# Kernel tuning notes

Hardware: AMD Instinct MI355X
Metric: run time of the kernel (lower is better)

Reference implementation:

```python
import jax, jax.numpy as jnp
import numpy as np

V, H, L, NH, DH, FF, P, T = 21128, 768, 12, 12, 64, 3072, 512, 9
B, S = 16, 256
EPS = 1e-12

def _ln(x, g, b):
    m = x.mean(-1, keepdims=True)
    v = ((x - m) ** 2).mean(-1, keepdims=True)
    return (x - m) * jax.lax.rsqrt(v + EPS) * g + b

def setup_inputs() -> dict:
    key = jax.random.key(0)
    ks = iter(jax.random.split(key, 64))
    def nrm(shape, s=0.02):
        return (jax.random.normal(next(ks), shape, jnp.float32) * s)
    inp = {
        'input_ids': jax.random.randint(next(ks), (B, 1, S), 0, V, dtype=jnp.int32),
        'token_type_ids': jnp.zeros((B, 1, S), jnp.int32),
        'attention_mask': jnp.ones((B, 1, S), jnp.int32),
        'tags': jax.random.randint(next(ks), (B, S), 0, T, dtype=jnp.int32),
        'word_emb': nrm((V, H)), 'pos_emb': nrm((P, H)), 'type_emb': nrm((2, H)),
        'emb_ln_g': jnp.ones((H,), jnp.float32), 'emb_ln_b': jnp.zeros((H,), jnp.float32),
        'Wq': nrm((L, H, H)), 'bq': jnp.zeros((L, H), jnp.float32),
        'Wk': nrm((L, H, H)), 'bk': jnp.zeros((L, H), jnp.float32),
        'Wv': nrm((L, H, H)), 'bv': jnp.zeros((L, H), jnp.float32),
        'Wo': nrm((L, H, H)), 'bo': jnp.zeros((L, H), jnp.float32),
        'ln1_g': jnp.ones((L, H), jnp.float32), 'ln1_b': jnp.zeros((L, H), jnp.float32),
        'W1': nrm((L, H, FF)), 'b1': jnp.zeros((L, FF), jnp.float32),
        'W2': nrm((L, FF, H)), 'b2': jnp.zeros((L, H), jnp.float32),
        'ln2_g': jnp.ones((L, H), jnp.float32), 'ln2_b': jnp.zeros((L, H), jnp.float32),
        'dense_W': nrm((H, T)), 'dense_b': jnp.zeros((T,), jnp.float32),
        'crf_start': nrm((T,), 0.1), 'crf_end': nrm((T,), 0.1), 'crf_trans': nrm((T, T), 0.1),
    }
    return inp

def _model(input_ids, token_type_ids, attention_mask, tags,
           word_emb, pos_emb, type_emb, emb_ln_g, emb_ln_b,
           Wq, bq, Wk, bk, Wv, bv, Wo, bo, ln1_g, ln1_b,
           W1, b1, W2, b2, ln2_g, ln2_b, dense_W, dense_b,
           crf_start, crf_end, crf_trans):
    ids = input_ids[:, 0, :]            # [B,S]
    tt = token_type_ids[:, 0, :]
    amask = attention_mask[:, 0, :]     # [B,S] int
    Bn, Sn = ids.shape
    # --- BERT embeddings (post-LN BERT-base) ---
    x = word_emb[ids] + pos_emb[:Sn][None, :, :] + type_emb[tt]
    x = _ln(x, emb_ln_g, emb_ln_b)
    bias = jnp.where(amask[:, None, None, :] > 0, 0.0, -1e9).astype(x.dtype)  # [B,1,1,S]
    scale = 1.0 / np.sqrt(DH).astype(np.float32)
    def layer(h, p):
        wq, bq_, wk, bk_, wv, bv_, wo, bo_, g1, c1, w1, d1, w2, d2, g2, c2 = p
        q = (h @ wq + bq_).reshape(Bn, Sn, NH, DH).transpose(0, 2, 1, 3)
        k = (h @ wk + bk_).reshape(Bn, Sn, NH, DH).transpose(0, 2, 1, 3)
        v = (h @ wv + bv_).reshape(Bn, Sn, NH, DH).transpose(0, 2, 1, 3)
        att = jax.nn.softmax(jnp.einsum('bhqd,bhkd->bhqk', q, k) * scale + bias, axis=-1)
        ctx = jnp.einsum('bhqk,bhkd->bhqd', att, v).transpose(0, 2, 1, 3).reshape(Bn, Sn, H)
        h = _ln(h + ctx @ wo + bo_, g1, c1)
        ff = jax.nn.gelu(h @ w1 + d1, approximate=False)
        h = _ln(h + ff @ w2 + d2, g2, c2)
        return h, None
    x, _ = jax.lax.scan(layer, x, (Wq, bq, Wk, bk, Wv, bv, Wo, bo, ln1_g, ln1_b, W1, b1, W2, b2, ln2_g, ln2_b))
    # --- emission head, seq-first like the torch code ---
    emis = (x @ dense_W + dense_b).transpose(1, 0, 2)   # [S,B,T]
    m = (amask.T > 0)                                    # [S,B] bool
    tags_sb = tags.T                                     # [S,B]
    bidx = jnp.arange(Bn)
    # --- CRF numerator (gold path score) ---
    score0 = crf_start[tags_sb[0]] + emis[0, bidx, tags_sb[0]]
    def num_step(sc, inp):
        e, t, tp, mm = inp
        inc = crf_trans[tp, t] + e[bidx, t]
        return sc + jnp.where(mm, inc, 0.0), None
    score, _ = jax.lax.scan(num_step, score0, (emis[1:], tags_sb[1:], tags_sb[:-1], m[1:]))
    lengths = m.astype(jnp.int32).sum(0)                 # [B]
    last_tag = jnp.take_along_axis(tags_sb, (lengths - 1)[None, :], axis=0)[0]
    score = score + crf_end[last_tag]
    # --- CRF partition (forward algorithm) ---
    alpha0 = crf_start[None, :] + emis[0]                # [B,T]
    def fwd_step(a, inp):
        e, mm = inp
        nxt = jax.nn.logsumexp(a[:, :, None] + crf_trans[None, :, :] + e[:, None, :], axis=1)
        return jnp.where(mm[:, None], nxt, a), None
    alpha, _ = jax.lax.scan(fwd_step, alpha0, (emis[1:], m[1:]))
    logZ = jax.nn.logsumexp(alpha + crf_end[None, :], axis=-1)
    loss = -(score - logZ).mean()                        # reduction='mean'
    # --- Viterbi decode ---
    v0 = crf_start[None, :] + emis[0]
    tid = jnp.arange(T)
    def vit_step(vv, inp):
        e, mm = inp
        sc = vv[:, :, None] + crf_trans[None, :, :]       # [B,T,T]
        nv = sc.max(1) + e
        idx = sc.argmax(1).astype(jnp.int32)
        vv2 = jnp.where(mm[:, None], nv, vv)
        idx = jnp.where(mm[:, None], idx, tid[None, :].astype(jnp.int32))
        return vv2, idx
    vfin, hist = jax.lax.scan(vit_step, v0, (emis[1:], m[1:]))  # hist: [S-1,B,T]
    last = jnp.argmax(vfin + crf_end[None, :], axis=-1).astype(jnp.int32)  # [B]
    def back_step(t, h):
        prev = jnp.take_along_axis(h, t[:, None], axis=1)[:, 0]
        return prev, prev
    _, path = jax.lax.scan(back_step, last, hist, reverse=True)  # [S-1,B]
    preds = jnp.concatenate([path, last[None, :]], axis=0).T     # [B,S]
    return loss, preds

def reference(input_ids, token_type_ids, attention_mask, tags,
              word_emb, pos_emb, type_emb, emb_ln_g, emb_ln_b,
              Wq, bq, Wk, bk, Wv, bv, Wo, bo, ln1_g, ln1_b,
              W1, b1, W2, b2, ln2_g, ln2_b, dense_W, dense_b,
              crf_start, crf_end, crf_trans):
    return _model(input_ids, token_type_ids, attention_mask, tags,
                  word_emb, pos_emb, type_emb, emb_ln_g, emb_ln_b,
                  Wq, bq, Wk, bk, Wv, bv, Wo, bo, ln1_g, ln1_b,
                  W1, b1, W2, b2, ln2_g, ln2_b, dense_W, dense_b,
                  crf_start, crf_end, crf_trans)
```

## Files before the change

### kernel.cpp

```cpp
#include <hip/hip_runtime.h>
#include <math.h>

#define B_ 16
#define S_ 256
#define H_ 768
#define L_ 12
#define NH_ 12
#define DH_ 64
#define FF_ 3072
#define T_ 9

typedef unsigned short ushort_t;
typedef __attribute__((ext_vector_type(8))) __bf16 bf16x8;
typedef __attribute__((ext_vector_type(4))) float f32x4;
typedef __attribute__((ext_vector_type(4))) unsigned short us4;
typedef __attribute__((ext_vector_type(4))) unsigned int u32x4;

__device__ __forceinline__ ushort_t f2bf(float f) {
  union { float f; unsigned u; } v; v.f = f;
  unsigned r = v.u + 0x7FFFu + ((v.u >> 16) & 1u);
  return (ushort_t)(r >> 16);
}
__device__ __forceinline__ float bf2f(ushort_t h) {
  union { unsigned u; float f; } v; v.u = ((unsigned)h) << 16;
  return v.f;
}
__device__ __forceinline__ void gload16(const void* g, void* l) {
  __builtin_amdgcn_global_load_lds((const __attribute__((address_space(1))) void*)g,
                                   (__attribute__((address_space(3))) void*)l, 16, 0, 0);
}

__global__ __launch_bounds__(256) void emb_ln_kernel(const int* __restrict__ ids, const int* __restrict__ tt,
                              const float* __restrict__ we, const float* __restrict__ pe,
                              const float* __restrict__ te, const float* __restrict__ g,
                              const float* __restrict__ bb, float* __restrict__ out,
                              ushort_t* __restrict__ oh, ushort_t* __restrict__ ol) {
  const int token = blockIdx.x;
  const int tid = threadIdx.x;
  const int s = token & (S_ - 1);
  const int id = ids[token];
  const int t2 = tt[token];
  float x[3];
  float sum = 0.f;
#pragma unroll
  for (int i = 0; i < 3; ++i) {
    int d = tid + i * 256;
    x[i] = we[(size_t)id * H_ + d] + pe[(size_t)s * H_ + d] + te[(size_t)t2 * H_ + d];
    sum += x[i];
  }
  __shared__ float red[4];
#pragma unroll
  for (int o = 32; o > 0; o >>= 1) sum += __shfl_xor(sum, o, 64);
  const int wid = tid >> 6, lane = tid & 63;
  if (lane == 0) red[wid] = sum;
  __syncthreads();
  const float mean = (red[0] + red[1] + red[2] + red[3]) * (1.f / H_);
  float vs = 0.f;
#pragma unroll
  for (int i = 0; i < 3; ++i) { float dv = x[i] - mean; vs += dv * dv; }
#pragma unroll
  for (int o = 32; o > 0; o >>= 1) vs += __shfl_xor(vs, o, 64);
  __syncthreads();
  if (lane == 0) red[wid] = vs;
  __syncthreads();
  const float var = (red[0] + red[1] + red[2] + red[3]) * (1.f / H_);
  const float inv = rsqrtf(var + 1e-12f);
  float* op = out + (size_t)token * H_;
  ushort_t* hp = oh + (size_t)token * H_;
  ushort_t* lp = ol + (size_t)token * H_;
#pragma unroll
  for (int i = 0; i < 3; ++i) {
    int d = tid + i * 256;
    float y = (x[i] - mean) * inv * g[d] + bb[d];
    op[d] = y;
    ushort_t h = f2bf(y);
    hp[d] = h;
    lp[d] = f2bf(y - bf2f(h));
  }
}

__global__ __launch_bounds__(256) void ln_kernel(const float* __restrict__ base, const float* __restrict__ delta,
                          const float* __restrict__ g, const float* __restrict__ bb,
                          float* __restrict__ out, ushort_t* __restrict__ oh, ushort_t* __restrict__ ol) {
  const int token = blockIdx.x;
  const int tid = threadIdx.x;
  const float* bp = base + (size_t)token * H_;
  const float* dp = delta + (size_t)token * H_;
  float x[3];
  float s = 0.f;
#pragma unroll
  for (int i = 0; i < 3; ++i) { int d = tid + i * 256; x[i] = bp[d] + dp[d]; s += x[i]; }
  __shared__ float red[4];
#pragma unroll
  for (int o = 32; o > 0; o >>= 1) s += __shfl_xor(s, o, 64);
  const int wid = tid >> 6, lane = tid & 63;
  if (lane == 0) red[wid] = s;
  __syncthreads();
  const float mean = (red[0] + red[1] + red[2] + red[3]) * (1.f / H_);
  float vs = 0.f;
#pragma unroll
  for (int i = 0; i < 3; ++i) { float dv = x[i] - mean; vs += dv * dv; }
#pragma unroll
  for (int o = 32; o > 0; o >>= 1) vs += __shfl_xor(vs, o, 64);
  __syncthreads();
  if (lane == 0) red[wid] = vs;
  __syncthreads();
  const float var = (red[0] + red[1] + red[2] + red[3]) * (1.f / H_);
  const float inv = rsqrtf(var + 1e-12f);
  float* op = out + (size_t)token * H_;
  ushort_t* hp = oh + (size_t)token * H_;
  ushort_t* lp = ol + (size_t)token * H_;
#pragma unroll
  for (int i = 0; i < 3; ++i) {
    int d = tid + i * 256;
    float y = (x[i] - mean) * inv * g[d] + bb[d];
    op[d] = y;
    ushort_t h = f2bf(y);
    hp[d] = h;
    lp[d] = f2bf(y - bf2f(h));
  }
}

__device__ __forceinline__ void transpose_core(float (*t)[65], const float* __restrict__ src,
                                               ushort_t* __restrict__ dh,
                                               int K, int N, int n0, int k0) {
  const int tid = threadIdx.x;
#pragma unroll
  for (int i = 0; i < 16; ++i) {
    int lin = tid + i * 256;
    int kk = lin >> 6, nn = lin & 63;
    t[kk][nn] = src[(size_t)(k0 + kk) * N + n0 + nn];
  }
  __syncthreads();
#pragma unroll
  for (int i = 0; i < 16; ++i) {
    int lin = tid + i * 256;
    int nn = lin >> 6, kk = lin & 63;
    dh[(size_t)(n0 + nn) * K + k0 + kk] = f2bf(t[kk][nn]);
  }
}

__device__ __forceinline__ void wprep_dispatch(float (*t)[65], int wid,
                        const float* Wq, const float* Wk, const float* Wv, const float* Wo,
                        const float* W1, const float* W2,
                        ushort_t* WT4h, ushort_t* W1th, ushort_t* W2th) {
  if (wid < 576) {
    const int z = wid / 144, r = wid - z * 144;
    const int x = r % 12, y = r / 12;
    const float* src = z == 0 ? Wq : (z == 1 ? Wk : (z == 2 ? Wv : Wo));
    transpose_core(t, src, WT4h + (size_t)z * H_ * H_, H_, H_, x * 64, y * 64);
  } else if (wid < 1152) {
    const int i = wid - 576;
    const int x = i % 48, y = i / 48;
    transpose_core(t, W1, W1th, H_, FF_, x * 64, y * 64);
  } else {
    const int i = wid - 1152;
    const int x = i % 12, y = i / 12;
    transpose_core(t, W2, W2th, FF_, H_, x * 64, y * 64);
  }
}

__global__ __launch_bounds__(256) void wprep_k(const float* __restrict__ Wq, const float* __restrict__ Wk,
                        const float* __restrict__ Wv, const float* __restrict__ Wo,
                        const float* __restrict__ W1, const float* __restrict__ W2,
                        ushort_t* __restrict__ WT4h,
                        ushort_t* __restrict__ W1th, ushort_t* __restrict__ W2th) {
  __shared__ float t[64][65];
  wprep_dispatch(t, blockIdx.x, Wq, Wk, Wv, Wo, W1, W2, WT4h, W1th, W2th);
}

template <int R>
__device__ __forceinline__ void stage_slice(const ushort_t* __restrict__ gsrc, int K, char* lds) {
  const int tid = threadIdx.x;
  constexpr int NIT = (R * 4) / 256;
#pragma unroll
  for (int i = 0; i < NIT; ++i) {
    const int v = tid + i * 256;
    const int kh = v / (2 * R);
    const int r2 = v & (2 * R - 1);
    const int row = r2 >> 1;
    const int kg = (kh << 1) | ((r2 & 1) ^ ((row >> 2) & 1));
    gload16(gsrc + (size_t)row * K + kg * 8, lds + (i * 256 + (tid & 192)) * 16);
  }
}
template <int R>
__device__ __forceinline__ void stage64(const ushort_t* __restrict__ gsrc, int K, char* lds) {
  stage_slice<R>(gsrc, K, lds);
  stage_slice<R>(gsrc + 32, K, lds + R * 64);
}

template <int BM, int BN>
__device__ __forceinline__ void mgemm_acc(
    const ushort_t* __restrict__ Ah, const ushort_t* __restrict__ Al,
    const ushort_t* __restrict__ Bth,
    int K, f32x4 (&acc)[BM / 32][BN / 32],
    ushort_t* sAh, ushort_t* sAl, ushort_t* sBh) {
  constexpr int FM = BM / 32;
  constexpr int FN = BN / 32;
  const int tid = threadIdx.x;
  const int w = tid >> 6, lane = tid & 63;
  const int wm = w >> 1, wn = w & 1;
  const int kgL = lane >> 4, lr = lane & 15;
  const int row0 = blockIdx.y * BM, col0 = blockIdx.x * BN;

#pragma unroll
  for (int i = 0; i < FM; ++i)
#pragma unroll
    for (int j = 0; j < FN; ++j) acc[i][j] = (f32x4){0.f, 0.f, 0.f, 0.f};

  const int khL = kgL >> 1;
  const int swz = (((kgL & 1) ^ ((lr >> 2) & 1)) << 4);
  const int aB0 = khL * (BM * 32) + (wm * (BM / 2) + lr) * 32 + swz;
  const int bB0 = khL * (BN * 32) + (wn * (BN / 2) + lr) * 32 + swz;

  const ushort_t* gA_h = Ah + (size_t)row0 * K;
  const ushort_t* gA_l = Al + (size_t)row0 * K;
  const ushort_t* gB_h = Bth + (size_t)col0 * K;

  for (int k0 = 0; k0 < K; k0 += 64) {
    stage64<BM>(gA_h + k0, K, (char*)sAh);
    stage64<BM>(gA_l + k0, K, (char*)sAl);
    stage64<BN>(gB_h + k0, K, (char*)sBh);
    __syncthreads();

#pragma unroll
    for (int ks = 0; ks < 2; ++ks) {
      const int ao = ks * BM * 64 + aB0;
      const int bo = ks * BN * 64 + bB0;
      bf16x8 a_h[FM], a_l[FM], b_h[FN];
#pragma unroll
      for (int fm = 0; fm < FM; ++fm) {
        a_h[fm] = *(const bf16x8*)((const char*)sAh + ao + fm * 512);
        a_l[fm] = *(const bf16x8*)((const char*)sAl + ao + fm * 512);
      }
#pragma unroll
      for (int fn = 0; fn < FN; ++fn) {
        b_h[fn] = *(const bf16x8*)((const char*)sBh + bo + fn * 512);
      }
#pragma unroll
      for (int fm = 0; fm < FM; ++fm)
#pragma unroll
        for (int fn = 0; fn < FN; ++fn) {
          f32x4 c = acc[fm][fn];
          c = __builtin_amdgcn_mfma_f32_16x16x32_bf16(a_h[fm], b_h[fn], c, 0, 0, 0);
          c = __builtin_amdgcn_mfma_f32_16x16x32_bf16(a_l[fm], b_h[fn], c, 0, 0, 0);
          acc[fm][fn] = c;
        }
    }
    __syncthreads();
  }
}

template <int BM, int BN, int EPI>
__global__ __launch_bounds__(256) void mgemm(const ushort_t* __restrict__ Ah, const ushort_t* __restrict__ Al,
                      const ushort_t* __restrict__ Bth,
                      const float* __restrict__ bias, float* __restrict__ Cf,
                      ushort_t* __restrict__ Ch, ushort_t* __restrict__ Cl, int N, int K) {
  __shared__ __attribute__((aligned(16))) ushort_t sAh[BM * 64];
  __shared__ __attribute__((aligned(16))) ushort_t sAl[BM * 64];
  __shared__ __attribute__((aligned(16))) ushort_t sBh[BN * 64];
  f32x4 acc[BM / 32][BN / 32];
  mgemm_acc<BM, BN>(Ah, Al, Bth, K, acc, sAh, sAl, sBh);
  const int tid = threadIdx.x;
  const int w = tid >> 6, lane = tid & 63;
  const int wm = w >> 1, wn = w & 1;
  const int kg = lane >> 4, lr = lane & 15;
  const int row0 = blockIdx.y * BM, col0 = blockIdx.x * BN;
#pragma unroll
  for (int fn = 0; fn < BN / 32; ++fn) {
    const int col = col0 + wn * (BN / 2) + fn * 16 + lr;
    const float bv = bias[col];
#pragma unroll
    for (int fm = 0; fm < BM / 32; ++fm) {
#pragma unroll
      for (int r = 0; r < 4; ++r) {
        const int row = row0 + wm * (BM / 2) + fm * 16 + kg * 4 + r;
        float v = acc[fm][fn][r] + bv;
        if (EPI == 0) {
          Cf[(size_t)row * N + col] = v;
        } else {
          float gl = 0.5f * v * (1.f + erff(v * 0.70710678118654752f));
          ushort_t h = f2bf(gl);
          Ch[(size_t)row * N + col] = h;
          Cl[(size_t)row * N + col] = f2bf(gl - bf2f(h));
        }
      }
    }
  }
}

__global__ __launch_bounds__(256) void ff1_fused(
    const ushort_t* __restrict__ Xh, const ushort_t* __restrict__ Xl,
    const ushort_t* __restrict__ W1th, const float* __restrict__ bias,
    ushort_t* __restrict__ Ch, ushort_t* __restrict__ Cl,
    const float* __restrict__ WqN, const float* __restrict__ WkN,
    const float* __restrict__ WvN, const float* __restrict__ WoN,
    const float* __restrict__ W1N, const float* __restrict__ W2N,
    ushort_t* __restrict__ WT4hN, ushort_t* __restrict__ W1thN, ushort_t* __restrict__ W2thN) {
  __shared__ __attribute__((aligned(16))) char pool[128 * 64 * 2 * 3];
  if (blockIdx.y >= 32) {
    if (WqN == nullptr) return;
    const int wid = (blockIdx.y - 32) * 24 + blockIdx.x;
    wprep_dispatch((float(*)[65])pool, wid, WqN, WkN, WvN, WoN, W1N, W2N, WT4hN, W1thN, W2thN);
    return;
  }
  ushort_t* sAh = (ushort_t*)pool;
  ushort_t* sAl = sAh + 128 * 64;
  ushort_t* sBh = sAl + 128 * 64;
  f32x4 acc[4][4];
  mgemm_acc<128, 128>(Xh, Xl, W1th, H_, acc, sAh, sAl, sBh);
  const int tid = threadIdx.x;
  const int w = tid >> 6, lane = tid & 63;
  const int wm = w >> 1, wn = w & 1;
  const int kg = lane >> 4, lr = lane & 15;
  const int row0 = blockIdx.y * 128, col0 = blockIdx.x * 128;
#pragma unroll
  for (int fn = 0; fn < 4; ++fn) {
    const int col = col0 + wn * 64 + fn * 16 + lr;
    const float bv = bias[col];
#pragma unroll
    for (int fm = 0; fm < 4; ++fm) {
#pragma unroll
      for (int r = 0; r < 4; ++r) {
        const int row = row0 + wm * 64 + fm * 16 + kg * 4 + r;
        float v = acc[fm][fn][r] + bv;
        float gl = 0.5f * v * (1.f + erff(v * 0.70710678118654752f));
        ushort_t h = f2bf(gl);
        Ch[(size_t)row * FF_ + col] = h;
        Cl[(size_t)row * FF_ + col] = f2bf(gl - bf2f(h));
      }
    }
  }
}

__global__ __launch_bounds__(256) void qkv_m(const ushort_t* __restrict__ Xh, const ushort_t* __restrict__ Xl,
                      const ushort_t* __restrict__ WT4h,
                      const float* __restrict__ bq, const float* __restrict__ bk,
                      const float* __restrict__ bvv,
                      ushort_t* __restrict__ Qh, ushort_t* __restrict__ Ql,
                      ushort_t* __restrict__ Kh, ushort_t* __restrict__ Vth) {
  __shared__ __attribute__((aligned(16))) ushort_t sAh[128 * 64];
  __shared__ __attribute__((aligned(16))) ushort_t sAl[128 * 64];
  __shared__ __attribute__((aligned(16))) ushort_t sBh[128 * 64];
  const int z = blockIdx.z;
  const ushort_t* Bh = WT4h + (size_t)z * H_ * H_;
  const float* bias = z == 0 ? bq : (z == 1 ? bk : bvv);
  f32x4 acc[4][4];
  mgemm_acc<128, 128>(Xh, Xl, Bh, H_, acc, sAh, sAl, sBh);
  const int tid = threadIdx.x;
  const int w = tid >> 6, lane = tid & 63;
  const int wm = w >> 1, wn = w & 1;
  const int kg = lane >> 4, lr = lane & 15;
  const int row0 = blockIdx.y * 128, col0 = blockIdx.x * 128;
#pragma unroll
  for (int fn = 0; fn < 4; ++fn) {
    const int col = col0 + wn * 64 + fn * 16 + lr;
    const float bv = bias[col];
#pragma unroll
    for (int fm = 0; fm < 4; ++fm) {
      const int rowb = row0 + wm * 64 + fm * 16 + kg * 4;
      if (z == 0) {
#pragma unroll
        for (int r = 0; r < 4; ++r) {
          float v = acc[fm][fn][r] + bv;
          ushort_t h = f2bf(v);
          Qh[(size_t)(rowb + r) * H_ + col] = h;
          Ql[(size_t)(rowb + r) * H_ + col] = f2bf(v - bf2f(h));
        }
      } else if (z == 1) {
#pragma unroll
        for (int r = 0; r < 4; ++r) {
          Kh[(size_t)(rowb + r) * H_ + col] = f2bf(acc[fm][fn][r] + bv);
        }
      } else {
        us4 h4;
#pragma unroll
        for (int r = 0; r < 4; ++r) h4[r] = f2bf(acc[fm][fn][r] + bv);
        const int bb2 = rowb >> 8, s0 = rowb & 255;
        const int hh2 = col >> 6, d = col & 63;
        *(us4*)(Vth + ((size_t)(bb2 * NH_ + hh2) * DH_ + d) * S_ + s0) = h4;
      }
    }
  }
}

__global__ __launch_bounds__(256, 3) void attn_mfma(
    const ushort_t* __restrict__ Qh, const ushort_t* __restrict__ Ql,
    const ushort_t* __restrict__ Kh, const ushort_t* __restrict__ Vth,
    const int* __restrict__ amask,
    ushort_t* __restrict__ Oh, ushort_t* __restrict__ Ol) {
  const int bid = blockIdx.x;
  const int qt = bid / 192;
  const int gh = bid - qt * 192;
  const int b = gh / NH_;
  const int h = gh - b * NH_;
  __shared__ __attribute__((aligned(16))) ushort_t sKh[64 * 64];
  __shared__ __attribute__((aligned(16))) ushort_t sVh[64 * 64];
  __shared__ __attribute__((aligned(16))) unsigned sP[4][16 * 68];
  __shared__ float sBias[64];
  const int tid = threadIdx.x;
  const int w = tid >> 6, lane = tid & 63;
  const int kg = lane >> 4, lr = lane & 15;

  const int qrow = b * S_ + qt * 64 + w * 16 + lr;
  bf16x8 qfh[2], qfl[2];
#pragma unroll
  for (int ds2 = 0; ds2 < 2; ++ds2) {
    const size_t off = (size_t)qrow * H_ + h * DH_ + ds2 * 32 + kg * 8;
    qfh[ds2] = *(const bf16x8*)(Qh + off);
    qfl[ds2] = *(const bf16x8*)(Ql + off);
  }

  f32x4 ctx[4];
#pragma unroll
  for (int i = 0; i < 4; ++i) ctx[i] = (f32x4){0.f, 0.f, 0.f, 0.f};
  float mrow[4], lrw[4];
#pragma unroll
  for (int r = 0; r < 4; ++r) { mrow[r] = -1e30f; lrw[r] = 0.f; }

  unsigned* sPw = &sP[w][0];

  for (int kt = 0; kt < 4; ++kt) {
#pragma unroll
    for (int i = 0; i < 2; ++i) {
      const int v = tid + i * 256;
      const int row = v >> 3;
      const int c16 = (v & 7) ^ (row & 7);
      const size_t kgl = (size_t)(b * S_ + kt * 64 + row) * H_ + h * DH_ + c16 * 8;
      gload16(Kh + kgl, (char*)sKh + v * 16);
      const size_t vgl = (size_t)((b * NH_ + h) * DH_ + row) * S_ + kt * 64 + c16 * 8;
      gload16(Vth + vgl, (char*)sVh + v * 16);
    }
    if (tid < 64) sBias[tid] = (amask[b * S_ + kt * 64 + tid] > 0) ? 0.f : -1e9f;
    __syncthreads();

    f32x4 sc[4];
#pragma unroll
    for (int kf = 0; kf < 4; ++kf) sc[kf] = (f32x4){0.f, 0.f, 0.f, 0.f};
#pragma unroll
    for (int kf = 0; kf < 4; ++kf) {
      const int krow = kf * 16 + lr;
#pragma unroll
      for (int ds2 = 0; ds2 < 2; ++ds2) {
        const int cb = (ds2 * 64 + kg * 16) ^ ((krow & 7) << 4);
        const bf16x8 kvh = *(const bf16x8*)((const char*)sKh + krow * 128 + cb);
        sc[kf] = __builtin_amdgcn_mfma_f32_16x16x32_bf16(qfh[ds2], kvh, sc[kf], 0, 0, 0);
        sc[kf] = __builtin_amdgcn_mfma_f32_16x16x32_bf16(qfl[ds2], kvh, sc[kf], 0, 0, 0);
      }
    }
    float bsv[4];
#pragma unroll
    for (int kf = 0; kf < 4; ++kf) bsv[kf] = sBias[kf * 16 + lr];

#pragma unroll
    for (int r = 0; r < 4; ++r) {
      float sv[4];
      float tmax = -1e30f;
#pragma unroll
      for (int kf = 0; kf < 4; ++kf) {
        sv[kf] = sc[kf][r] * 0.125f + bsv[kf];
        tmax = fmaxf(tmax, sv[kf]);
      }
#pragma unroll
      for (int o = 8; o > 0; o >>= 1) tmax = fmaxf(tmax, __shfl_xor(tmax, o, 64));
      const float mnew = fmaxf(mrow[r], tmax);
      const float corr = expf(mrow[r] - mnew);
      float ls = 0.f;
      const int qoff = (kg * 4 + r) * 68;
#pragma unroll
      for (int kf = 0; kf < 4; ++kf) {
        const float pe = expf(sv[kf] - mnew);
        ls += pe;
        const ushort_t hi = f2bf(pe);
        const ushort_t lo = f2bf(pe - bf2f(hi));
        sPw[qoff + kf * 16 + lr] = ((unsigned)hi << 16) | lo;
      }
#pragma unroll
      for (int o = 8; o > 0; o >>= 1) ls += __shfl_xor(ls, o, 64);
      lrw[r] = lrw[r] * corr + ls;
      mrow[r] = mnew;
#pragma unroll
      for (int df = 0; df < 4; ++df) ctx[df][r] *= corr;
    }

#pragma unroll
    for (int ks = 0; ks < 2; ++ks) {
      unsigned w8[8];
      *(u32x4*)&w8[0] = *(const u32x4*)(sPw + lr * 68 + ks * 32 + kg * 8);
      *(u32x4*)&w8[4] = *(const u32x4*)(sPw + lr * 68 + ks * 32 + kg * 8 + 4);
      union { bf16x8 v; ushort_t u[8]; } ph, pl;
#pragma unroll
      for (int j = 0; j < 8; ++j) { ph.u[j] = (ushort_t)(w8[j] >> 16); pl.u[j] = (ushort_t)(w8[j] & 0xffffu); }
#pragma unroll
      for (int df = 0; df < 4; ++df) {
        const int vrow = df * 16 + lr;
        const int cb = (ks * 64 + kg * 16) ^ ((vrow & 7) << 4);
        const bf16x8 vvh = *(const bf16x8*)((const char*)sVh + vrow * 128 + cb);
        ctx[df] = __builtin_amdgcn_mfma_f32_16x16x32_bf16(ph.v, vvh, ctx[df], 0, 0, 0);
        ctx[df] = __builtin_amdgcn_mfma_f32_16x16x32_bf16(pl.v, vvh, ctx[df], 0, 0, 0);
      }
    }
    __syncthreads();
  }

#pragma unroll
  for (int r = 0; r < 4; ++r) {
    const float inv = 1.f / lrw[r];
    const int tok = b * S_ + qt * 64 + w * 16 + kg * 4 + r;
#pragma unroll
    for (int df = 0; df < 4; ++df) {
      const float v = ctx[df][r] * inv;
      const ushort_t hi = f2bf(v);
      const size_t o = (size_t)tok * H_ + h * DH_ + df * 16 + lr;
      Oh[o] = hi;
      Ol[o] = f2bf(v - bf2f(hi));
    }
  }
}

__global__ __launch_bounds__(256) void emis_kernel(const float* __restrict__ X, const float* __restrict__ W,
                            const float* __restrict__ bias, float* __restrict__ E) {
  const int wave = (blockIdx.x * 256 + threadIdx.x) >> 6;
  const int lane = threadIdx.x & 63;
  const int b = wave >> 8, s = wave & 255;
  const float* xp = X + (size_t)wave * H_;
  float acc[T_];
#pragma unroll
  for (int t = 0; t < T_; ++t) acc[t] = 0.f;
  for (int i = 0; i < 12; ++i) {
    const int d = lane + i * 64;
    const float xv = xp[d];
    const float* wp = W + (size_t)d * T_;
#pragma unroll
    for (int t = 0; t < T_; ++t) acc[t] = fmaf(xv, wp[t], acc[t]);
  }
#pragma unroll
  for (int t = 0; t < T_; ++t) {
    float v = acc[t];
#pragma unroll
    for (int o = 32; o > 0; o >>= 1) v += __shfl_xor(v, o, 64);
    acc[t] = v;
  }
  if (lane < T_) E[((size_t)s * B_ + b) * T_ + lane] = acc[lane] + bias[lane];
}

__global__ __launch_bounds__(128) void crf_kernel(const float* __restrict__ emis, const int* __restrict__ tags,
                          const int* __restrict__ amask,
                          const float* __restrict__ crf_start, const float* __restrict__ crf_end,
                          const float* __restrict__ trans,
                          float* __restrict__ partial, float* __restrict__ out) {
  const int b = blockIdx.x;
  const int tid = threadIdx.x;
  const int wv = tid >> 6;
  const int lane = tid & 63;
  __shared__ float sE[S_ * T_];
  __shared__ float sM[S_];
  __shared__ float trs[T_ * T_];
  __shared__ unsigned char hist[S_ - 1][16];
  __shared__ float pathf[S_];
  for (int i = tid; i < S_ * T_; i += 128) {
    const int s = i / T_, t = i - s * T_;
    sE[i] = emis[((size_t)s * B_ + b) * T_ + t];
  }
  for (int i = tid; i < S_; i += 128) sM[i] = (float)amask[b * S_ + i];
  for (int i = tid; i < T_ * T_; i += 128) trs[i] = trans[i];
  __syncthreads();

  const int t = lane;
  const bool act = t < T_;
  float trc[T_];
#pragma unroll
  for (int p = 0; p < T_; ++p) trc[p] = act ? trs[p * T_ + t] : 0.f;

  if (wv == 0) {
    float alpha = act ? crf_start[t] + sE[t] : 0.f;
    for (int s = 1; s < S_; ++s) {
      float ap[T_];
#pragma unroll
      for (int p = 0; p < T_; ++p) ap[p] = __shfl(alpha, p, 64);
      if (act) {
        const float e = sE[s * T_ + t];
        float mx = -1e30f;
#pragma unroll
        for (int p = 0; p < T_; ++p) mx = fmaxf(mx, ap[p] + trc[p]);
        float sum = 0.f;
#pragma unroll
        for (int p = 0; p < T_; ++p) sum += __expf(ap[p] + trc[p] - mx);
        const float na = mx + __logf(sum) + e;
        if (sM[s] > 0.f) alpha = na;
      }
    }
    float nsum = 0.f;
    int len = 0;
#pragma unroll
    for (int j = 0; j < 4; ++j) {
      const int s = lane + j * 64;
      const int mk = (sM[s] > 0.f) ? 1 : 0;
      len += mk;
      if (s >= 1 && mk) {
        const int tc = tags[b * S_ + s], tp = tags[b * S_ + s - 1];
        nsum += trs[tp * T_ + tc] + sE[s * T_ + tc];
      }
    }
#pragma unroll
    for (int o = 32; o > 0; o >>= 1) {
      nsum += __shfl_xor(nsum, o, 64);
      len += __shfl_xor(len, o, 64);
    }
    const float fz = act ? alpha + crf_end[t] : -1e30f;
    float zp[T_];
#pragma unroll
    for (int p = 0; p < T_; ++p) zp[p] = __shfl(fz, p, 64);
    if (lane == 0) {
      float mx = -1e30f;
#pragma unroll
      for (int p = 0; p < T_; ++p) mx = fmaxf(mx, zp[p]);
      float sum = 0.f;
#pragma unroll
      for (int p = 0; p < T_; ++p) sum += __expf(zp[p] - mx);
      const float logZ = mx + __logf(sum);
      const int tg0 = tags[b * S_];
      const float score = nsum + crf_start[tg0] + sE[tg0] + crf_end[tags[b * S_ + len - 1]];
      partial[b] = score - logZ;
    }
  } else {
    float vit = act ? crf_start[t] + sE[t] : 0.f;
    for (int s = 1; s < S_; ++s) {
      float vp[T_];
#pragma unroll
      for (int p = 0; p < T_; ++p) vp[p] = __shfl(vit, p, 64);
      if (act) {
        const float e = sE[s * T_ + t];
        float best = -1e30f; int bi = 0;
#pragma unroll
        for (int p = 0; p < T_; ++p) {
          const float scv = vp[p] + trc[p];
          if (scv > best) { best = scv; bi = p; }
        }
        if (sM[s] > 0.f) {
          vit = best + e;
          hist[s - 1][t] = (unsigned char)bi;
        } else {
          hist[s - 1][t] = (unsigned char)t;
        }
      }
    }
    const float fv = act ? vit + crf_end[t] : -1e30f;
    float wp[T_];
#pragma unroll
    for (int p = 0; p < T_; ++p) wp[p] = __shfl(fv, p, 64);
    if (lane == 0) {
      float best = -1e30f; int lastTag = 0;
#pragma unroll
      for (int p = 0; p < T_; ++p) {
        if (wp[p] > best) { best = wp[p]; lastTag = p; }
      }
      int tc = lastTag;
      pathf[S_ - 1] = (float)tc;
      for (int i = S_ - 2; i >= 0; --i) {
        tc = hist[i][tc];
        pathf[i] = (float)tc;
      }
    }
  }
  __syncthreads();
#pragma unroll
  for (int j = 0; j < 2; ++j) {
    const int s = tid + j * 128;
    out[1 + b * S_ + s] = pathf[s];
  }
}

__global__ __launch_bounds__(64) void crf_final(const float* __restrict__ partial, float* __restrict__ out) {
  const int lane = threadIdx.x;
  float v = (lane < B_) ? partial[lane] : 0.f;
#pragma unroll
  for (int o = 32; o > 0; o >>= 1) v += __shfl_xor(v, o, 64);
  if (lane == 0) out[0] = -(v * (1.f / B_));
}

extern "C" void kernel_launch(void* const* d_in, const int* in_sizes, int n_in,
                              void* d_out, int out_size, void* d_ws, size_t ws_size,
                              hipStream_t stream) {
  const int* input_ids = (const int*)d_in[0];
  const int* token_type_ids = (const int*)d_in[1];
  const int* attention_mask = (const int*)d_in[2];
  const int* tags = (const int*)d_in[3];
  const float* word_emb = (const float*)d_in[4];
  const float* pos_emb = (const float*)d_in[5];
  const float* type_emb = (const float*)d_in[6];
  const float* emb_ln_g = (const float*)d_in[7];
  const float* emb_ln_b = (const float*)d_in[8];
  const float* Wq = (const float*)d_in[9];
  const float* bq = (const float*)d_in[10];
  const float* Wk = (const float*)d_in[11];
  const float* bk = (const float*)d_in[12];
  const float* Wv = (const float*)d_in[13];
  const float* bv = (const float*)d_in[14];
  const float* Wo = (const float*)d_in[15];
  const float* bo = (const float*)d_in[16];
  const float* ln1_g = (const float*)d_in[17];
  const float* ln1_b = (const float*)d_in[18];
  const float* W1 = (const float*)d_in[19];
  const float* b1 = (const float*)d_in[20];
  const float* W2 = (const float*)d_in[21];
  const float* b2 = (const float*)d_in[22];
  const float* ln2_g = (const float*)d_in[23];
  const float* ln2_b = (const float*)d_in[24];
  const float* dense_W = (const float*)d_in[25];
  const float* dense_b = (const float*)d_in[26];
  const float* crf_start = (const float*)d_in[27];
  const float* crf_end = (const float*)d_in[28];
  const float* crf_trans = (const float*)d_in[29];

  constexpr size_t NTOK = (size_t)B_ * S_;
  constexpr size_t XSZ = NTOK * H_;
  constexpr size_t WT4SZ = (size_t)4 * H_ * H_;
  constexpr size_t WFSZ = (size_t)H_ * FF_;

  char* p = (char*)d_ws;
  float* X = (float*)p;            p += XSZ * 4;
  float* TMP = (float*)p;          p += XSZ * 4;
  char* UN = p;                    p += 8 * XSZ * 2;
  ushort_t* Qh = (ushort_t*)UN;
  ushort_t* Ql = Qh + XSZ;
  ushort_t* Kh = Ql + XSZ;
  ushort_t* Vth = Kh + XSZ;
  ushort_t* CTXh = Vth + XSZ;
  ushort_t* CTXl = CTXh + XSZ;
  ushort_t* FFh = (ushort_t*)UN;
  ushort_t* FFl = FFh + NTOK * FF_;
  ushort_t* Xh = (ushort_t*)p;     p += XSZ * 2;
  ushort_t* Xl = (ushort_t*)p;     p += XSZ * 2;
  ushort_t* WT4h2 = (ushort_t*)p;  p += WT4SZ * 2 * 2;
  ushort_t* W1th2 = (ushort_t*)p;  p += WFSZ * 2 * 2;
  ushort_t* W2th2 = (ushort_t*)p;  p += WFSZ * 2 * 2;
  float* EM = (float*)p;           p += (size_t)S_ * B_ * T_ * 4;
  float* PART = (float*)p;         p += B_ * 4;

  emb_ln_kernel<<<dim3(4096), dim3(256), 0, stream>>>(input_ids, token_type_ids, word_emb, pos_emb,
                                                      type_emb, emb_ln_g, emb_ln_b, X, Xh, Xl);
  wprep_k<<<dim3(1728), dim3(256), 0, stream>>>(Wq, Wk, Wv, Wo, W1, W2, WT4h2, W1th2, W2th2);

  for (int l = 0; l < L_; ++l) {
    const int pr = l & 1, pn = (l + 1) & 1;
    ushort_t* WT4h = WT4h2 + (size_t)pr * WT4SZ;
    ushort_t* W1th = W1th2 + (size_t)pr * WFSZ;
    ushort_t* W2th = W2th2 + (size_t)pr * WFSZ;
    const bool hasNext = (l + 1 < L_);
    const size_t wo_n = (size_t)(l + 1) * H_ * H_;

    qkv_m<<<dim3(6, 32, 3), dim3(256), 0, stream>>>(Xh, Xl, WT4h, bq + (size_t)l * H_,
                                                    bk + (size_t)l * H_, bv + (size_t)l * H_,
                                                    Qh, Ql, Kh, Vth);
    attn_mfma<<<dim3(768), dim3(256), 0, stream>>>(Qh, Ql, Kh, Vth, attention_mask, CTXh, CTXl);
    mgemm<64, 64, 0><<<dim3(12, 64), dim3(256), 0, stream>>>(
        CTXh, CTXl, WT4h + (size_t)3 * H_ * H_,
        bo + (size_t)l * H_, TMP, nullptr, nullptr, H_, H_);
    ln_kernel<<<dim3(4096), dim3(256), 0, stream>>>(X, TMP, ln1_g + (size_t)l * H_,
                                                    ln1_b + (size_t)l * H_, X, Xh, Xl);
    ff1_fused<<<dim3(24, 32 + 72), dim3(256), 0, stream>>>(
        Xh, Xl, W1th, b1 + (size_t)l * FF_, FFh, FFl,
        hasNext ? Wq + wo_n : nullptr, Wk + wo_n, Wv + wo_n, Wo + wo_n,
        W1 + (size_t)(l + 1) * WFSZ, W2 + (size_t)(l + 1) * WFSZ,
        WT4h2 + (size_t)pn * WT4SZ, W1th2 + (size_t)pn * WFSZ, W2th2 + (size_t)pn * WFSZ);
    mgemm<64, 64, 0><<<dim3(12, 64), dim3(256), 0, stream>>>(
        FFh, FFl, W2th, b2 + (size_t)l * H_, TMP, nullptr, nullptr, H_, FF_);
    ln_kernel<<<dim3(4096), dim3(256), 0, stream>>>(X, TMP, ln2_g + (size_t)l * H_,
                                                    ln2_b + (size_t)l * H_, X, Xh, Xl);
  }

  emis_kernel<<<dim3(1024), dim3(256), 0, stream>>>(X, dense_W, dense_b, EM);
  crf_kernel<<<dim3(B_), dim3(128), 0, stream>>>(EM, tags, attention_mask, crf_start, crf_end,
                                                 crf_trans, PART, (float*)d_out);
  crf_final<<<dim3(1), dim3(64), 0, stream>>>(PART, (float*)d_out);
}
```

Before: 3.420 ms.

## Double-buffer LDS staging in GEMM and attention kernels with manual vmcnt waits

Adds double-buffered shared-memory staging to the GEMM core and the attention K/V loop: the next tile's global-to-LDS loads are issued before computing on the current tile, with explicit s_waitcnt vmcnt and raw barriers in place of __syncthreads. The 128x128 GEMMs drop to a 32-deep K tile so the double buffer fits in 48KB, and launch bounds request 3 blocks per CU. The aim is to overlap global memory latency with MFMA work. Hard-coded vmcnt counts are fragile and must match the number of loads per stage. The smaller K tile also means more barriers per K.

```diff
diff --git a/kernel.cpp b/kernel.cpp
--- a/kernel.cpp
+++ b/kernel.cpp
@@ -183,20 +183,17 @@
     gload16(gsrc + (size_t)row * K + kg * 8, lds + (i * 256 + (tid & 192)) * 16);
   }
 }
-template <int R>
-__device__ __forceinline__ void stage64(const ushort_t* __restrict__ gsrc, int K, char* lds) {
-  stage_slice<R>(gsrc, K, lds);
-  stage_slice<R>(gsrc + 32, K, lds + R * 64);
-}
-
-template <int BM, int BN>
+
+template <int BM, int BN, int BK>
 __device__ __forceinline__ void mgemm_acc(
     const ushort_t* __restrict__ Ah, const ushort_t* __restrict__ Al,
     const ushort_t* __restrict__ Bth,
-    int K, f32x4 (&acc)[BM / 32][BN / 32],
-    ushort_t* sAh, ushort_t* sAl, ushort_t* sBh) {
+    int K, f32x4 (&acc)[BM / 32][BN / 32], char* pool) {
   constexpr int FM = BM / 32;
   constexpr int FN = BN / 32;
+  constexpr int ABYTES = BM * BK * 2;
+  constexpr int BBYTES = BN * BK * 2;
+  constexpr int BUF = 2 * ABYTES + BBYTES;
   const int tid = threadIdx.x;
   const int w = tid >> 6, lane = tid & 63;
   const int wm = w >> 1, wn = w & 1;
@@ -217,25 +214,41 @@
   const ushort_t* gA_l = Al + (size_t)row0 * K;
   const ushort_t* gB_h = Bth + (size_t)col0 * K;
 
-  for (int k0 = 0; k0 < K; k0 += 64) {
-    stage64<BM>(gA_h + k0, K, (char*)sAh);
-    stage64<BM>(gA_l + k0, K, (char*)sAl);
-    stage64<BN>(gB_h + k0, K, (char*)sBh);
-    __syncthreads();
-
-#pragma unroll
-    for (int ks = 0; ks < 2; ++ks) {
-      const int ao = ks * BM * 64 + aB0;
-      const int bo = ks * BN * 64 + bB0;
+  auto stageall = [&](int k0, char* buf) {
+#pragma unroll
+    for (int c = 0; c < BK / 32; ++c) {
+      stage_slice<BM>(gA_h + k0 + c * 32, K, buf + c * BM * 64);
+      stage_slice<BM>(gA_l + k0 + c * 32, K, buf + ABYTES + c * BM * 64);
+      stage_slice<BN>(gB_h + k0 + c * 32, K, buf + 2 * ABYTES + c * BN * 64);
+    }
+  };
+
+  const int nk = K / BK;
+  stageall(0, pool);
+  for (int k = 0; k < nk; ++k) {
+    char* cur = pool + (k & 1) * BUF;
+    if (k + 1 < nk) {
+      stageall((k + 1) * BK, pool + ((k + 1) & 1) * BUF);
+      asm volatile("s_waitcnt vmcnt(6)" ::: "memory");
+    } else {
+      asm volatile("s_waitcnt vmcnt(0)" ::: "memory");
+    }
+    __builtin_amdgcn_s_barrier();
+    asm volatile("" ::: "memory");
+
+#pragma unroll
+    for (int ks = 0; ks < BK / 32; ++ks) {
+      const char* aP = cur + ks * BM * 64;
+      const char* bP = cur + 2 * ABYTES + ks * BN * 64;
       bf16x8 a_h[FM], a_l[FM], b_h[FN];
 #pragma unroll
       for (int fm = 0; fm < FM; ++fm) {
-        a_h[fm] = *(const bf16x8*)((const char*)sAh + ao + fm * 512);
-        a_l[fm] = *(const bf16x8*)((const char*)sAl + ao + fm * 512);
+        a_h[fm] = *(const bf16x8*)(aP + aB0 + fm * 512);
+        a_l[fm] = *(const bf16x8*)(aP + ABYTES + aB0 + fm * 512);
       }
 #pragma unroll
       for (int fn = 0; fn < FN; ++fn) {
-        b_h[fn] = *(const bf16x8*)((const char*)sBh + bo + fn * 512);
+        b_h[fn] = *(const bf16x8*)(bP + bB0 + fn * 512);
       }
 #pragma unroll
       for (int fm = 0; fm < FM; ++fm)
@@ -247,20 +260,19 @@
           acc[fm][fn] = c;
         }
     }
-    __syncthreads();
-  }
-}
-
-template <int BM, int BN, int EPI>
-__global__ __launch_bounds__(256) void mgemm(const ushort_t* __restrict__ Ah, const ushort_t* __restrict__ Al,
+    asm volatile("" ::: "memory");
+    __builtin_amdgcn_s_barrier();
+  }
+}
+
+template <int BM, int BN, int BK, int EPI>
+__global__ __launch_bounds__(256, 3) void mgemm(const ushort_t* __restrict__ Ah, const ushort_t* __restrict__ Al,
                       const ushort_t* __restrict__ Bth,
                       const float* __restrict__ bias, float* __restrict__ Cf,
                       ushort_t* __restrict__ Ch, ushort_t* __restrict__ Cl, int N, int K) {
-  __shared__ __attribute__((aligned(16))) ushort_t sAh[BM * 64];
-  __shared__ __attribute__((aligned(16))) ushort_t sAl[BM * 64];
-  __shared__ __attribute__((aligned(16))) ushort_t sBh[BN * 64];
+  __shared__ __attribute__((aligned(16))) char pool[2 * (2 * BM * BK + BN * BK) * 2];
   f32x4 acc[BM / 32][BN / 32];
-  mgemm_acc<BM, BN>(Ah, Al, Bth, K, acc, sAh, sAl, sBh);
+  mgemm_acc<BM, BN, BK>(Ah, Al, Bth, K, acc, pool);
   const int tid = threadIdx.x;
   const int w = tid >> 6, lane = tid & 63;
   const int wm = w >> 1, wn = w & 1;
@@ -289,7 +301,7 @@
   }
 }
 
-__global__ __launch_bounds__(256) void ff1_fused(
+__global__ __launch_bounds__(256, 3) void ff1_fused(
     const ushort_t* __restrict__ Xh, const ushort_t* __restrict__ Xl,
     const ushort_t* __restrict__ W1th, const float* __restrict__ bias,
     ushort_t* __restrict__ Ch, ushort_t* __restrict__ Cl,
@@ -297,18 +309,15 @@
     const float* __restrict__ WvN, const float* __restrict__ WoN,
     const float* __restrict__ W1N, const float* __restrict__ W2N,
     ushort_t* __restrict__ WT4hN, ushort_t* __restrict__ W1thN, ushort_t* __restrict__ W2thN) {
-  __shared__ __attribute__((aligned(16))) char pool[128 * 64 * 2 * 3];
+  __shared__ __attribute__((aligned(16))) char pool[49152];
   if (blockIdx.y >= 32) {
     if (WqN == nullptr) return;
     const int wid = (blockIdx.y - 32) * 24 + blockIdx.x;
     wprep_dispatch((float(*)[65])pool, wid, WqN, WkN, WvN, WoN, W1N, W2N, WT4hN, W1thN, W2thN);
     return;
   }
-  ushort_t* sAh = (ushort_t*)pool;
-  ushort_t* sAl = sAh + 128 * 64;
-  ushort_t* sBh = sAl + 128 * 64;
   f32x4 acc[4][4];
-  mgemm_acc<128, 128>(Xh, Xl, W1th, H_, acc, sAh, sAl, sBh);
+  mgemm_acc<128, 128, 32>(Xh, Xl, W1th, H_, acc, pool);
   const int tid = threadIdx.x;
   const int w = tid >> 6, lane = tid & 63;
   const int wm = w >> 1, wn = w & 1;
@@ -333,20 +342,18 @@
   }
 }
 
-__global__ __launch_bounds__(256) void qkv_m(const ushort_t* __restrict__ Xh, const ushort_t* __restrict__ Xl,
+__global__ __launch_bounds__(256, 3) void qkv_m(const ushort_t* __restrict__ Xh, const ushort_t* __restrict__ Xl,
                       const ushort_t* __restrict__ WT4h,
                       const float* __restrict__ bq, const float* __restrict__ bk,
                       const float* __restrict__ bvv,
                       ushort_t* __restrict__ Qh, ushort_t* __restrict__ Ql,
                       ushort_t* __restrict__ Kh, ushort_t* __restrict__ Vth) {
-  __shared__ __attribute__((aligned(16))) ushort_t sAh[128 * 64];
-  __shared__ __attribute__((aligned(16))) ushort_t sAl[128 * 64];
-  __shared__ __attribute__((aligned(16))) ushort_t sBh[128 * 64];
+  __shared__ __attribute__((aligned(16))) char pool[49152];
   const int z = blockIdx.z;
   const ushort_t* Bh = WT4h + (size_t)z * H_ * H_;
   const float* bias = z == 0 ? bq : (z == 1 ? bk : bvv);
   f32x4 acc[4][4];
-  mgemm_acc<128, 128>(Xh, Xl, Bh, H_, acc, sAh, sAl, sBh);
+  mgemm_acc<128, 128, 32>(Xh, Xl, Bh, H_, acc, pool);
   const int tid = threadIdx.x;
   const int w = tid >> 6, lane = tid & 63;
   const int wm = w >> 1, wn = w & 1;
@@ -394,10 +401,10 @@
   const int gh = bid - qt * 192;
   const int b = gh / NH_;
   const int h = gh - b * NH_;
-  __shared__ __attribute__((aligned(16))) ushort_t sKh[64 * 64];
-  __shared__ __attribute__((aligned(16))) ushort_t sVh[64 * 64];
+  __shared__ __attribute__((aligned(16))) ushort_t sKh[2][64 * 64];
+  __shared__ __attribute__((aligned(16))) ushort_t sVh[2][64 * 64];
   __shared__ __attribute__((aligned(16))) unsigned sP[4][16 * 68];
-  __shared__ float sBias[64];
+  __shared__ float sBias[2][64];
   const int tid = threadIdx.x;
   const int w = tid >> 6, lane = tid & 63;
   const int kg = lane >> 4, lr = lane & 15;
@@ -420,19 +427,31 @@
 
   unsigned* sPw = &sP[w][0];
 
-  for (int kt = 0; kt < 4; ++kt) {
+  auto stageKV = [&](int kt, int bufi) {
 #pragma unroll
     for (int i = 0; i < 2; ++i) {
       const int v = tid + i * 256;
       const int row = v >> 3;
       const int c16 = (v & 7) ^ (row & 7);
       const size_t kgl = (size_t)(b * S_ + kt * 64 + row) * H_ + h * DH_ + c16 * 8;
-      gload16(Kh + kgl, (char*)sKh + v * 16);
+      gload16(Kh + kgl, (char*)&sKh[bufi][0] + v * 16);
       const size_t vgl = (size_t)((b * NH_ + h) * DH_ + row) * S_ + kt * 64 + c16 * 8;
-      gload16(Vth + vgl, (char*)sVh + v * 16);
-    }
-    if (tid < 64) sBias[tid] = (amask[b * S_ + kt * 64 + tid] > 0) ? 0.f : -1e9f;
-    __syncthreads();
+      gload16(Vth + vgl, (char*)&sVh[bufi][0] + v * 16);
+    }
+    if (tid < 64) sBias[bufi][tid] = (amask[b * S_ + kt * 64 + tid] > 0) ? 0.f : -1e9f;
+  };
+
+  stageKV(0, 0);
+  for (int kt = 0; kt < 4; ++kt) {
+    const int bi = kt & 1;
+    if (kt < 3) {
+      stageKV(kt + 1, bi ^ 1);
+      asm volatile("s_waitcnt vmcnt(4) lgkmcnt(0)" ::: "memory");
+    } else {
+      asm volatile("s_waitcnt vmcnt(0) lgkmcnt(0)" ::: "memory");
+    }
+    __builtin_amdgcn_s_barrier();
+    asm volatile("" ::: "memory");
 
     f32x4 sc[4];
 #pragma unroll
@@ -443,14 +462,14 @@
 #pragma unroll
       for (int ds2 = 0; ds2 < 2; ++ds2) {
         const int cb = (ds2 * 64 + kg * 16) ^ ((krow & 7) << 4);
-        const bf16x8 kvh = *(const bf16x8*)((const char*)sKh + krow * 128 + cb);
+        const bf16x8 kvh = *(const bf16x8*)((const char*)&sKh[bi][0] + krow * 128 + cb);
         sc[kf] = __builtin_amdgcn_mfma_f32_16x16x32_bf16(qfh[ds2], kvh, sc[kf], 0, 0, 0);
         sc[kf] = __builtin_amdgcn_mfma_f32_16x16x32_bf16(qfl[ds2], kvh, sc[kf], 0, 0, 0);
       }
     }
     float bsv[4];
 #pragma unroll
-    for (int kf = 0; kf < 4; ++kf) bsv[kf] = sBias[kf * 16 + lr];
+    for (int kf = 0; kf < 4; ++kf) bsv[kf] = sBias[bi][kf * 16 + lr];
 
 #pragma unroll
     for (int r = 0; r < 4; ++r) {
@@ -495,12 +514,13 @@
       for (int df = 0; df < 4; ++df) {
         const int vrow = df * 16 + lr;
         const int cb = (ks * 64 + kg * 16) ^ ((vrow & 7) << 4);
-        const bf16x8 vvh = *(const bf16x8*)((const char*)sVh + vrow * 128 + cb);
+        const bf16x8 vvh = *(const bf16x8*)((const char*)&sVh[bi][0] + vrow * 128 + cb);
         ctx[df] = __builtin_amdgcn_mfma_f32_16x16x32_bf16(ph.v, vvh, ctx[df], 0, 0, 0);
         ctx[df] = __builtin_amdgcn_mfma_f32_16x16x32_bf16(pl.v, vvh, ctx[df], 0, 0, 0);
       }
     }
-    __syncthreads();
+    asm volatile("" ::: "memory");
+    __builtin_amdgcn_s_barrier();
   }
 
 #pragma unroll
@@ -754,7 +774,7 @@
                                                     bk + (size_t)l * H_, bv + (size_t)l * H_,
                                                     Qh, Ql, Kh, Vth);
     attn_mfma<<<dim3(768), dim3(256), 0, stream>>>(Qh, Ql, Kh, Vth, attention_mask, CTXh, CTXl);
-    mgemm<64, 64, 0><<<dim3(12, 64), dim3(256), 0, stream>>>(
+    mgemm<64, 64, 64, 0><<<dim3(12, 64), dim3(256), 0, stream>>>(
         CTXh, CTXl, WT4h + (size_t)3 * H_ * H_,
         bo + (size_t)l * H_, TMP, nullptr, nullptr, H_, H_);
     ln_kernel<<<dim3(4096), dim3(256), 0, stream>>>(X, TMP, ln1_g + (size_t)l * H_,
@@ -764,7 +784,7 @@
         hasNext ? Wq + wo_n : nullptr, Wk + wo_n, Wv + wo_n, Wo + wo_n,
         W1 + (size_t)(l + 1) * WFSZ, W2 + (size_t)(l + 1) * WFSZ,
         WT4h2 + (size_t)pn * WT4SZ, W1th2 + (size_t)pn * WFSZ, W2th2 + (size_t)pn * WFSZ);
-    mgemm<64, 64, 0><<<dim3(12, 64), dim3(256), 0, stream>>>(
+    mgemm<64, 64, 64, 0><<<dim3(12, 64), dim3(256), 0, stream>>>(
         FFh, FFl, W2th, b2 + (size_t)l * H_, TMP, nullptr, nullptr, H_, FF_);
     ln_kernel<<<dim3(4096), dim3(256), 0, stream>>>(X, TMP, ln2_g + (size_t)l * H_,
                                                     ln2_b + (size_t)l * H_, X, Xh, Xl);
```

New measurement: 3.385 ms. About the same (-1.0%).
